# Kernel optimization log

Measured on AMD Instinct MI355X. Metric: run time of the kernel, lower is better.

Reference implementation:

```python
import jax, jax.numpy as jnp
import numpy as np

N = 50000          # nodes
E = 800000         # edges (avg degree 16)
INPUT_DIM = 1024
K = 10             # conv1d kernel
STRIDE = 8
COUT = (INPUT_DIM - K) // STRIDE + 1   # 127, matches floor formula
H = 256            # hidden_dim


def setup_inputs() -> dict:
    key = jax.random.key(0)
    ks = jax.random.split(key, 12)
    sc = lambda k, s: (jax.random.normal(k, s, jnp.float32) * 0.05)
    inp = {}
    inp["h"] = jax.random.normal(ks[0], (N, INPUT_DIM), jnp.float32)
    inp["src"] = jax.random.randint(ks[1], (E,), 0, N, dtype=jnp.int32)
    inp["dst"] = jax.random.randint(ks[2], (E,), 0, N, dtype=jnp.int32)
    # Conv1d(1,1,k=10,stride=8)
    inp["conv1d_w"] = sc(ks[3], (1, 1, K))
    inp["conv1d_b"] = jnp.zeros((1,), jnp.float32)
    # SAGEConv1: 127 -> 256 (mean aggregator: fc_self + fc_neigh)
    inp["w_self1"] = sc(ks[4], (COUT, H))
    inp["w_neigh1"] = sc(ks[5], (COUT, H))
    inp["b1"] = jnp.zeros((H,), jnp.float32)
    # SAGEConv2: 256 -> 128
    inp["w_self2"] = sc(ks[6], (H, H // 2))
    inp["w_neigh2"] = sc(ks[7], (H, H // 2))
    inp["b2"] = jnp.zeros((H // 2,), jnp.float32)
    # MLP head 128 -> 64 -> 32 -> 1
    inp["fc1_w"] = sc(ks[8], (H // 2, H // 4)); inp["fc1_b"] = jnp.zeros((H // 4,), jnp.float32)
    inp["fc2_w"] = sc(ks[9], (H // 4, H // 8)); inp["fc2_b"] = jnp.zeros((H // 8,), jnp.float32)
    inp["fc3_w"] = sc(ks[10], (H // 8, 1));    inp["fc3_b"] = jnp.zeros((1,), jnp.float32)
    return inp


def _sage_mean(x, src, dst, w_self, w_neigh, b):
    # mean over in-neighbors (src -> dst), zero for isolated nodes (DGL semantics)
    ones = jnp.ones((src.shape[0],), x.dtype)
    deg = jax.ops.segment_sum(ones, dst, num_segments=N)          # [N]
    agg = jax.ops.segment_sum(x[src], dst, num_segments=N)        # [N, F]
    agg = agg / jnp.maximum(deg, 1.0)[:, None]
    return x @ w_self + agg @ w_neigh + b


def reference(h, src, dst, conv1d_w, conv1d_b,
              w_self1, w_neigh1, b1, w_self2, w_neigh2, b2,
              fc1_w, fc1_b, fc2_w, fc2_b, fc3_w, fc3_b):
    # per-node 1D conv over feature axis: [N,1,1024] -> [N,1,127]
    x = jax.lax.conv_general_dilated(h[:, None, :], conv1d_w, (STRIDE,), 'VALID',
                                     dimension_numbers=('NCH', 'OIH', 'NCH'))
    x = jax.nn.relu(x[:, 0, :] + conv1d_b)                        # [N, 127]
    x = jax.nn.relu(_sage_mean(x, src, dst, w_self1, w_neigh1, b1))  # [N, 256]
    x = jax.nn.relu(_sage_mean(x, src, dst, w_self2, w_neigh2, b2))  # [N, 128]
    hg = jnp.mean(x, axis=0, keepdims=True)                       # AvgPooling -> [1, 128]
    y = jax.nn.relu(hg @ fc1_w + fc1_b)
    y = jax.nn.relu(y @ fc2_w + fc2_b)
    return y @ fc3_w + fc3_b                                      # [1, 1]
```

## Files before the change

kernel.cpp:

```cpp
#include <hip/hip_runtime.h>

#define N_NODES 50000
#define N_EDGES 800000
#define IN_DIM  1024
#define COUT    127
#define H1      256
#define H2      128
#define LDA     256
#define MBLK    391
#define NPART   4096
#define LDSS    72

typedef __bf16 bf16;
typedef __attribute__((ext_vector_type(8))) __bf16 bf16x8;
typedef __attribute__((ext_vector_type(4))) float floatx4;

__global__ void conv_kernel(const float* __restrict__ h, const float* __restrict__ w,
                            const float* __restrict__ b, bf16* __restrict__ xa) {
    int n = blockIdx.x;
    int t = threadIdx.x;
    const float* hr = h + (size_t)n * IN_DIM;
    float r = 0.f;
    if (t < COUT) {
        const float* p = hr + t * 8;
        float4 a = *(const float4*)p;
        float4 c = *(const float4*)(p + 4);
        float2 d = *(const float2*)(p + 8);
        float s = b[0];
        s += a.x * w[0] + a.y * w[1] + a.z * w[2] + a.w * w[3];
        s += c.x * w[4] + c.y * w[5] + c.z * w[6] + c.w * w[7];
        s += d.x * w[8] + d.y * w[9];
        r = fmaxf(s, 0.f);
    }
    xa[(size_t)n * LDA + t] = (bf16)r;
}

__global__ void deg_kernel(const int* __restrict__ dst, int* __restrict__ deg) {
    int e = blockIdx.x * blockDim.x + threadIdx.x;
    if (e < N_EDGES) atomicAdd(&deg[dst[e]], 1);
}

__global__ __launch_bounds__(1024) void scan_kernel(const int* __restrict__ deg,
                                                    int* __restrict__ rowptr,
                                                    int* __restrict__ cursor) {
    __shared__ int wsum[16];
    __shared__ int carry_s;
    int tid = threadIdx.x;
    int lane = tid & 63, wid = tid >> 6;
    if (tid == 0) carry_s = 0;
    __syncthreads();
    for (int base = 0; base < N_NODES; base += 1024) {
        int i = base + tid;
        int v = (i < N_NODES) ? deg[i] : 0;
        int s = v;
        #pragma unroll
        for (int off = 1; off < 64; off <<= 1) {
            int t = __shfl_up(s, off);
            if (lane >= off) s += t;
        }
        if (lane == 63) wsum[wid] = s;
        __syncthreads();
        if (tid < 16) {
            int ws = wsum[tid];
            #pragma unroll
            for (int off = 1; off < 16; off <<= 1) {
                int t = __shfl_up(ws, off);
                if (tid >= off) ws += t;
            }
            wsum[tid] = ws;
        }
        __syncthreads();
        int wpre = (wid == 0) ? 0 : wsum[wid - 1];
        int excl = carry_s + wpre + (s - v);
        if (i < N_NODES) { rowptr[i] = excl; cursor[i] = excl; }
        int tot = wsum[15];
        __syncthreads();
        if (tid == 0) carry_s += tot;
        __syncthreads();
    }
    if (tid == 0) rowptr[N_NODES] = carry_s;
}

__global__ void fill_kernel(const int* __restrict__ src, const int* __restrict__ dst,
                            int* __restrict__ cursor, int* __restrict__ esrc) {
    int e = blockIdx.x * blockDim.x + threadIdx.x;
    if (e < N_EDGES) {
        int d = dst[e];
        int pos = atomicAdd(&cursor[d], 1);
        esrc[pos] = src[e];
    }
}

__global__ void agg_kernel(bf16* __restrict__ xa, const int* __restrict__ rowptr,
                           const int* __restrict__ esrc) {
    int n = blockIdx.x;
    int f = threadIdx.x;
    int s0 = rowptr[n], s1 = rowptr[n + 1];
    float acc = 0.f;
    int e = s0;
    for (; e + 8 <= s1; e += 8) {
        int i0 = esrc[e],     i1 = esrc[e + 1], i2 = esrc[e + 2], i3 = esrc[e + 3];
        int i4 = esrc[e + 4], i5 = esrc[e + 5], i6 = esrc[e + 6], i7 = esrc[e + 7];
        float v0 = (float)xa[(size_t)i0 * LDA + f];
        float v1 = (float)xa[(size_t)i1 * LDA + f];
        float v2 = (float)xa[(size_t)i2 * LDA + f];
        float v3 = (float)xa[(size_t)i3 * LDA + f];
        float v4 = (float)xa[(size_t)i4 * LDA + f];
        float v5 = (float)xa[(size_t)i5 * LDA + f];
        float v6 = (float)xa[(size_t)i6 * LDA + f];
        float v7 = (float)xa[(size_t)i7 * LDA + f];
        acc += ((v0 + v1) + (v2 + v3)) + ((v4 + v5) + (v6 + v7));
    }
    for (; e < s1; ++e) acc += (float)xa[(size_t)esrc[e] * LDA + f];
    float dnm = (float)max(s1 - s0, 1);
    xa[(size_t)n * LDA + 128 + f] = (bf16)(acc / dnm);
}

__global__ void padw1_kernel(const float* __restrict__ ws, const float* __restrict__ wn,
                             bf16* __restrict__ wt) {
    int i = blockIdx.x * blockDim.x + threadIdx.x;
    int n = i >> 8, k = i & 255;
    float v = 0.f;
    if (k < COUT)                      v = ws[k * H1 + n];
    else if (k >= 128 && k < 128 + COUT) v = wn[(k - 128) * H1 + n];
    wt[i] = (bf16)v;
}

__global__ void padw2_kernel(const float* __restrict__ ws, const float* __restrict__ wn,
                             bf16* __restrict__ wt) {
    int i = blockIdx.x * blockDim.x + threadIdx.x;
    int n = i >> 8, k = i & 255;
    float v = (n < H2) ? ws[k * H2 + n] : wn[k * H2 + (n - H2)];
    wt[i] = (bf16)v;
}

template <bool RELU>
__global__ __launch_bounds__(256) void gemm_mfma(
        const bf16* __restrict__ X, const bf16* __restrict__ WT,
        const float* __restrict__ bias, bf16* __restrict__ out) {
    __shared__ bf16 As[128 * LDSS];
    __shared__ bf16 Bs[64 * LDSS];
    int tid  = threadIdx.x;
    int lane = tid & 63, w = tid >> 6;
    int quad = lane >> 4, l16 = lane & 15;
    int m0 = blockIdx.x * 128;
    int n0 = blockIdx.y * 64;
    floatx4 acc[2][4] = {};

    for (int k0 = 0; k0 < 256; k0 += 64) {
        uint4 av[4], bv[2];
        #pragma unroll
        for (int i = 0; i < 4; ++i) {
            int c = tid + 256 * i;
            int row = c >> 3, col = (c & 7) * 8;
            int gr = m0 + row;
            av[i] = (gr < N_NODES) ? *(const uint4*)(X + (size_t)gr * LDA + k0 + col)
                                   : make_uint4(0u, 0u, 0u, 0u);
        }
        #pragma unroll
        for (int i = 0; i < 2; ++i) {
            int c = tid + 256 * i;
            int row = c >> 3, col = (c & 7) * 8;
            bv[i] = *(const uint4*)(WT + (size_t)(n0 + row) * 256 + k0 + col);
        }
        __syncthreads();
        #pragma unroll
        for (int i = 0; i < 4; ++i) {
            int c = tid + 256 * i;
            int row = c >> 3, col = (c & 7) * 8;
            *(uint4*)&As[row * LDSS + col] = av[i];
        }
        #pragma unroll
        for (int i = 0; i < 2; ++i) {
            int c = tid + 256 * i;
            int row = c >> 3, col = (c & 7) * 8;
            *(uint4*)&Bs[row * LDSS + col] = bv[i];
        }
        __syncthreads();

        #pragma unroll
        for (int ks = 0; ks < 2; ++ks) {
            int kin = ks * 32 + quad * 8;
            bf16x8 a0 = *(const bf16x8*)&As[(w * 32 + l16) * LDSS + kin];
            bf16x8 a1 = *(const bf16x8*)&As[(w * 32 + 16 + l16) * LDSS + kin];
            bf16x8 b0 = *(const bf16x8*)&Bs[(l16) * LDSS + kin];
            bf16x8 b1 = *(const bf16x8*)&Bs[(16 + l16) * LDSS + kin];
            bf16x8 b2 = *(const bf16x8*)&Bs[(32 + l16) * LDSS + kin];
            bf16x8 b3 = *(const bf16x8*)&Bs[(48 + l16) * LDSS + kin];
            acc[0][0] = __builtin_amdgcn_mfma_f32_16x16x32_bf16(a0, b0, acc[0][0], 0, 0, 0);
            acc[0][1] = __builtin_amdgcn_mfma_f32_16x16x32_bf16(a0, b1, acc[0][1], 0, 0, 0);
            acc[0][2] = __builtin_amdgcn_mfma_f32_16x16x32_bf16(a0, b2, acc[0][2], 0, 0, 0);
            acc[0][3] = __builtin_amdgcn_mfma_f32_16x16x32_bf16(a0, b3, acc[0][3], 0, 0, 0);
            acc[1][0] = __builtin_amdgcn_mfma_f32_16x16x32_bf16(a1, b0, acc[1][0], 0, 0, 0);
            acc[1][1] = __builtin_amdgcn_mfma_f32_16x16x32_bf16(a1, b1, acc[1][1], 0, 0, 0);
            acc[1][2] = __builtin_amdgcn_mfma_f32_16x16x32_bf16(a1, b2, acc[1][2], 0, 0, 0);
            acc[1][3] = __builtin_amdgcn_mfma_f32_16x16x32_bf16(a1, b3, acc[1][3], 0, 0, 0);
        }
    }

    float bvv[4] = {};
    if constexpr (RELU) {
        #pragma unroll
        for (int nt = 0; nt < 4; ++nt) bvv[nt] = bias[n0 + nt * 16 + l16];
    }
    #pragma unroll
    for (int mt = 0; mt < 2; ++mt) {
        #pragma unroll
        for (int r = 0; r < 4; ++r) {
            int m = m0 + w * 32 + mt * 16 + quad * 4 + r;
            if (m < N_NODES) {
                #pragma unroll
                for (int nt = 0; nt < 4; ++nt) {
                    float v = acc[mt][nt][r];
                    if constexpr (RELU) v = fmaxf(v + bvv[nt], 0.f);
                    out[(size_t)m * LDA + n0 + nt * 16 + l16] = (bf16)v;
                }
            }
        }
    }
}

__global__ __launch_bounds__(128) void agg_epi_kernel(
        const bf16* __restrict__ P, const int* __restrict__ rowptr,
        const int* __restrict__ esrc, const float* __restrict__ b2,
        float* __restrict__ partial) {
    int f = threadIdx.x;
    float bf = b2[f];
    float csum = 0.f;
    for (int n = blockIdx.x; n < N_NODES; n += gridDim.x) {
        int s0 = rowptr[n], s1 = rowptr[n + 1];
        float acc = 0.f;
        int e = s0;
        for (; e + 8 <= s1; e += 8) {
            int i0 = esrc[e],     i1 = esrc[e + 1], i2 = esrc[e + 2], i3 = esrc[e + 3];
            int i4 = esrc[e + 4], i5 = esrc[e + 5], i6 = esrc[e + 6], i7 = esrc[e + 7];
            float v0 = (float)P[(size_t)i0 * LDA + H2 + f];
            float v1 = (float)P[(size_t)i1 * LDA + H2 + f];
            float v2 = (float)P[(size_t)i2 * LDA + H2 + f];
            float v3 = (float)P[(size_t)i3 * LDA + H2 + f];
            float v4 = (float)P[(size_t)i4 * LDA + H2 + f];
            float v5 = (float)P[(size_t)i5 * LDA + H2 + f];
            float v6 = (float)P[(size_t)i6 * LDA + H2 + f];
            float v7 = (float)P[(size_t)i7 * LDA + H2 + f];
            acc += ((v0 + v1) + (v2 + v3)) + ((v4 + v5) + (v6 + v7));
        }
        for (; e < s1; ++e) acc += (float)P[(size_t)esrc[e] * LDA + H2 + f];
        float dnm = (float)max(s1 - s0, 1);
        float y = (float)P[(size_t)n * LDA + f] + acc / dnm + bf;
        csum += fmaxf(y, 0.f);
    }
    partial[(size_t)blockIdx.x * 128 + f] = csum;
}

__global__ __launch_bounds__(256) void reduce_kernel(const float* __restrict__ partial,
                                                     float* __restrict__ hg) {
    int f = blockIdx.x, t = threadIdx.x;
    float s = 0.f;
    for (int i = t; i < NPART; i += 256) s += partial[(size_t)i * 128 + f];
    __shared__ float ls[4];
    #pragma unroll
    for (int off = 32; off >= 1; off >>= 1) s += __shfl_down(s, off);
    if ((t & 63) == 0) ls[t >> 6] = s;
    __syncthreads();
    if (t == 0) hg[f] = (ls[0] + ls[1]) + (ls[2] + ls[3]);
}

__global__ void mlp_kernel(const float* __restrict__ hg,
                           const float* __restrict__ f1w, const float* __restrict__ f1b,
                           const float* __restrict__ f2w, const float* __restrict__ f2b,
                           const float* __restrict__ f3w, const float* __restrict__ f3b,
                           float* __restrict__ out) {
    __shared__ float h0[128], y1[64], y2[32];
    int t = threadIdx.x;
    if (t < 128) h0[t] = hg[t] * (1.0f / N_NODES);
    __syncthreads();
    if (t < 64) {
        float s = f1b[t];
        for (int k = 0; k < 128; ++k) s += h0[k] * f1w[k * 64 + t];
        y1[t] = fmaxf(s, 0.f);
    }
    __syncthreads();
    if (t < 32) {
        float s = f2b[t];
        for (int k = 0; k < 64; ++k) s += y1[k] * f2w[k * 32 + t];
        y2[t] = fmaxf(s, 0.f);
    }
    __syncthreads();
    if (t == 0) {
        float s = f3b[0];
        for (int k = 0; k < 32; ++k) s += y2[k] * f3w[k];
        out[0] = s;
    }
}

extern "C" void kernel_launch(void* const* d_in, const int* in_sizes, int n_in,
                              void* d_out, int out_size, void* d_ws, size_t ws_size,
                              hipStream_t stream) {
    (void)in_sizes; (void)n_in; (void)out_size; (void)ws_size;
    const float* h        = (const float*)d_in[0];
    const int*   src      = (const int*)d_in[1];
    const int*   dst      = (const int*)d_in[2];
    const float* cw       = (const float*)d_in[3];
    const float* cb       = (const float*)d_in[4];
    const float* w_self1  = (const float*)d_in[5];
    const float* w_neigh1 = (const float*)d_in[6];
    const float* b1       = (const float*)d_in[7];
    const float* w_self2  = (const float*)d_in[8];
    const float* w_neigh2 = (const float*)d_in[9];
    const float* b2       = (const float*)d_in[10];
    const float* f1w      = (const float*)d_in[11];
    const float* f1b      = (const float*)d_in[12];
    const float* f2w      = (const float*)d_in[13];
    const float* f2b      = (const float*)d_in[14];
    const float* f3w      = (const float*)d_in[15];
    const float* f3b      = (const float*)d_in[16];
    float* out = (float*)d_out;

    char* ws = (char*)d_ws;
    bf16*  xa    = (bf16*) (ws + 0);
    bf16*  P     = (bf16*) (ws + 0);
    bf16*  x2    = (bf16*) (ws + 25624576);
    bf16*  wt1   = (bf16*) (ws + 51249152);
    bf16*  wt2   = (bf16*) (ws + 51380224);
    int*   deg   = (int*)  (ws + 51511296);
    int*   rowp  = (int*)  (ws + 51711488);
    int*   esrc  = (int*)  (ws + 51911936);
    float* part  = (float*)(ws + 55111936);
    float* hg    = (float*)(ws + 57209088);
    int*   cur   = deg;

    hipMemsetAsync(deg, 0, N_NODES * sizeof(int), stream);

    padw1_kernel<<<256, 256, 0, stream>>>(w_self1, w_neigh1, wt1);
    padw2_kernel<<<256, 256, 0, stream>>>(w_self2, w_neigh2, wt2);
    deg_kernel<<<(N_EDGES + 255) / 256, 256, 0, stream>>>(dst, deg);
    scan_kernel<<<1, 1024, 0, stream>>>(deg, rowp, cur);
    fill_kernel<<<(N_EDGES + 255) / 256, 256, 0, stream>>>(src, dst, cur, esrc);
    conv_kernel<<<N_NODES, 128, 0, stream>>>(h, cw, cb, xa);
    agg_kernel<<<N_NODES, 128, 0, stream>>>(xa, rowp, esrc);
    dim3 g(MBLK, 4);
    gemm_mfma<true><<<g, 256, 0, stream>>>(xa, wt1, b1, x2);
    gemm_mfma<false><<<g, 256, 0, stream>>>(x2, wt2, nullptr, P);
    agg_epi_kernel<<<NPART, 128, 0, stream>>>(P, rowp, esrc, b2, part);
    reduce_kernel<<<128, 256, 0, stream>>>(part, hg);
    mlp_kernel<<<1, 128, 0, stream>>>(hg, f1w, f1b, f2w, f2b, f3w, f3b, out);
}
```

Before: 599.9 us.

## Vectorize gathers to bf16x2 per lane, persist conv, fuse padw+memset, vectorize scan

Both neighbor-aggregation kernels now assign one wavefront per node, with each lane loading a packed pair of bf16 values and unpacking them with bit operations. This halves the gather instruction count, and readfirstlane keeps the row bounds scalar. The conv kernel becomes grid-stride with weights held in registers. The two weight-padding kernels and the degree memset are merged into one launch, and the scan processes 8 elements per thread using int4 loads and stores. The partial-sum buffer grows to 8192 rows, so the hg offset in the workspace moves.

Result: faster. 553.1 us (-7.8%).

```diff
diff --git a/kernel.cpp b/kernel.cpp
--- a/kernel.cpp
+++ b/kernel.cpp
@@ -8,31 +8,63 @@
 #define H2      128
 #define LDA     256
 #define MBLK    391
-#define NPART   4096
+#define EPB     2048
+#define NROWS   8192
 #define LDSS    72
 
 typedef __bf16 bf16;
 typedef __attribute__((ext_vector_type(8))) __bf16 bf16x8;
+typedef __attribute__((ext_vector_type(2))) __bf16 bf16x2;
 typedef __attribute__((ext_vector_type(4))) float floatx4;
 
-__global__ void conv_kernel(const float* __restrict__ h, const float* __restrict__ w,
-                            const float* __restrict__ b, bf16* __restrict__ xa) {
-    int n = blockIdx.x;
-    int t = threadIdx.x;
-    const float* hr = h + (size_t)n * IN_DIM;
-    float r = 0.f;
-    if (t < COUT) {
-        const float* p = hr + t * 8;
-        float4 a = *(const float4*)p;
-        float4 c = *(const float4*)(p + 4);
-        float2 d = *(const float2*)(p + 8);
-        float s = b[0];
-        s += a.x * w[0] + a.y * w[1] + a.z * w[2] + a.w * w[3];
-        s += c.x * w[4] + c.y * w[5] + c.z * w[6] + c.w * w[7];
-        s += d.x * w[8] + d.y * w[9];
-        r = fmaxf(s, 0.f);
-    }
-    xa[(size_t)n * LDA + t] = (bf16)r;
+__device__ __forceinline__ float blo(unsigned int u) { return __uint_as_float(u << 16); }
+__device__ __forceinline__ float bhi(unsigned int u) { return __uint_as_float(u & 0xffff0000u); }
+
+__global__ __launch_bounds__(256) void conv_kernel(const float* __restrict__ h,
+                                                   const float* __restrict__ w,
+                                                   const float* __restrict__ b,
+                                                   bf16* __restrict__ xa) {
+    int t    = threadIdx.x & 127;
+    int half = threadIdx.x >> 7;
+    float wv[10];
+    #pragma unroll
+    for (int j = 0; j < 10; ++j) wv[j] = w[j];
+    float bb = b[0];
+    for (int n = blockIdx.x * 2 + half; n < N_NODES; n += gridDim.x * 2) {
+        const float* hr = h + (size_t)n * IN_DIM;
+        float r = 0.f;
+        if (t < COUT) {
+            const float* p = hr + t * 8;
+            float4 a = *(const float4*)p;
+            float4 c = *(const float4*)(p + 4);
+            float2 d = *(const float2*)(p + 8);
+            float s = bb;
+            s += a.x * wv[0] + a.y * wv[1] + a.z * wv[2] + a.w * wv[3];
+            s += c.x * wv[4] + c.y * wv[5] + c.z * wv[6] + c.w * wv[7];
+            s += d.x * wv[8] + d.y * wv[9];
+            r = fmaxf(s, 0.f);
+        }
+        xa[(size_t)n * LDA + t] = (bf16)r;
+    }
+}
+
+__global__ void padw_kernel(const float* __restrict__ ws1, const float* __restrict__ wn1,
+                            const float* __restrict__ ws2, const float* __restrict__ wn2,
+                            bf16* __restrict__ wt1, bf16* __restrict__ wt2,
+                            int* __restrict__ deg) {
+    int i = blockIdx.x * blockDim.x + threadIdx.x;
+    int j = i & 65535;
+    int n = j >> 8, k = j & 255;
+    if (i < 65536) {
+        float v = 0.f;
+        if (k < COUT)                        v = ws1[k * H1 + n];
+        else if (k >= 128 && k < 128 + COUT) v = wn1[(k - 128) * H1 + n];
+        wt1[j] = (bf16)v;
+    } else {
+        float v = (n < H2) ? ws2[k * H2 + n] : wn2[k * H2 + (n - H2)];
+        wt2[j] = (bf16)v;
+    }
+    if (i < 50048) deg[i] = 0;
 }
 
 __global__ void deg_kernel(const int* __restrict__ dst, int* __restrict__ deg) {
@@ -49,10 +81,22 @@
     int lane = tid & 63, wid = tid >> 6;
     if (tid == 0) carry_s = 0;
     __syncthreads();
-    for (int base = 0; base < N_NODES; base += 1024) {
-        int i = base + tid;
-        int v = (i < N_NODES) ? deg[i] : 0;
-        int s = v;
+    for (int base = 0; base < N_NODES; base += 8192) {
+        int i0 = base + tid * 8;
+        int v[8];
+        if (i0 + 8 <= N_NODES) {
+            int4 a = *(const int4*)&deg[i0];
+            int4 c = *(const int4*)&deg[i0 + 4];
+            v[0] = a.x; v[1] = a.y; v[2] = a.z; v[3] = a.w;
+            v[4] = c.x; v[5] = c.y; v[6] = c.z; v[7] = c.w;
+        } else {
+            #pragma unroll
+            for (int j = 0; j < 8; ++j) v[j] = (i0 + j < N_NODES) ? deg[i0 + j] : 0;
+        }
+        int p[8]; int run = 0;
+        #pragma unroll
+        for (int j = 0; j < 8; ++j) { run += v[j]; p[j] = run; }
+        int s = run;
         #pragma unroll
         for (int off = 1; off < 64; off <<= 1) {
             int t = __shfl_up(s, off);
@@ -70,9 +114,20 @@
             wsum[tid] = ws;
         }
         __syncthreads();
-        int wpre = (wid == 0) ? 0 : wsum[wid - 1];
-        int excl = carry_s + wpre + (s - v);
-        if (i < N_NODES) { rowptr[i] = excl; cursor[i] = excl; }
+        int wpre  = (wid == 0) ? 0 : wsum[wid - 1];
+        int excl0 = carry_s + wpre + (s - run);
+        int o[8];
+        #pragma unroll
+        for (int j = 0; j < 8; ++j) o[j] = excl0 + p[j] - v[j];
+        if (i0 + 8 <= N_NODES) {
+            *(int4*)&rowptr[i0]     = make_int4(o[0], o[1], o[2], o[3]);
+            *(int4*)&rowptr[i0 + 4] = make_int4(o[4], o[5], o[6], o[7]);
+            *(int4*)&cursor[i0]     = make_int4(o[0], o[1], o[2], o[3]);
+            *(int4*)&cursor[i0 + 4] = make_int4(o[4], o[5], o[6], o[7]);
+        } else {
+            for (int j = 0; j < 8; ++j)
+                if (i0 + j < N_NODES) { rowptr[i0 + j] = o[j]; cursor[i0 + j] = o[j]; }
+        }
         int tot = wsum[15];
         __syncthreads();
         if (tid == 0) carry_s += tot;
@@ -91,47 +146,41 @@
     }
 }
 
-__global__ void agg_kernel(bf16* __restrict__ xa, const int* __restrict__ rowptr,
-                           const int* __restrict__ esrc) {
-    int n = blockIdx.x;
-    int f = threadIdx.x;
-    int s0 = rowptr[n], s1 = rowptr[n + 1];
-    float acc = 0.f;
+__global__ __launch_bounds__(256) void agg_kernel(bf16* __restrict__ xa,
+                                                  const int* __restrict__ rowptr,
+                                                  const int* __restrict__ esrc) {
+    int lane = threadIdx.x & 63;
+    int w    = threadIdx.x >> 6;
+    int n    = blockIdx.x * 4 + w;
+    int s0 = __builtin_amdgcn_readfirstlane(rowptr[n]);
+    int s1 = __builtin_amdgcn_readfirstlane(rowptr[n + 1]);
+    float ax = 0.f, ay = 0.f;
     int e = s0;
     for (; e + 8 <= s1; e += 8) {
         int i0 = esrc[e],     i1 = esrc[e + 1], i2 = esrc[e + 2], i3 = esrc[e + 3];
         int i4 = esrc[e + 4], i5 = esrc[e + 5], i6 = esrc[e + 6], i7 = esrc[e + 7];
-        float v0 = (float)xa[(size_t)i0 * LDA + f];
-        float v1 = (float)xa[(size_t)i1 * LDA + f];
-        float v2 = (float)xa[(size_t)i2 * LDA + f];
-        float v3 = (float)xa[(size_t)i3 * LDA + f];
-        float v4 = (float)xa[(size_t)i4 * LDA + f];
-        float v5 = (float)xa[(size_t)i5 * LDA + f];
-        float v6 = (float)xa[(size_t)i6 * LDA + f];
-        float v7 = (float)xa[(size_t)i7 * LDA + f];
-        acc += ((v0 + v1) + (v2 + v3)) + ((v4 + v5) + (v6 + v7));
-    }
-    for (; e < s1; ++e) acc += (float)xa[(size_t)esrc[e] * LDA + f];
+        unsigned u0 = ((const unsigned*)(xa + (size_t)i0 * LDA))[lane];
+        unsigned u1 = ((const unsigned*)(xa + (size_t)i1 * LDA))[lane];
+        unsigned u2 = ((const unsigned*)(xa + (size_t)i2 * LDA))[lane];
+        unsigned u3 = ((const unsigned*)(xa + (size_t)i3 * LDA))[lane];
+        unsigned u4 = ((const unsigned*)(xa + (size_t)i4 * LDA))[lane];
+        unsigned u5 = ((const unsigned*)(xa + (size_t)i5 * LDA))[lane];
+        unsigned u6 = ((const unsigned*)(xa + (size_t)i6 * LDA))[lane];
+        unsigned u7 = ((const unsigned*)(xa + (size_t)i7 * LDA))[lane];
+        ax += ((blo(u0) + blo(u1)) + (blo(u2) + blo(u3)))
+            + ((blo(u4) + blo(u5)) + (blo(u6) + blo(u7)));
+        ay += ((bhi(u0) + bhi(u1)) + (bhi(u2) + bhi(u3)))
+            + ((bhi(u4) + bhi(u5)) + (bhi(u6) + bhi(u7)));
+    }
+    for (; e < s1; ++e) {
+        unsigned u = ((const unsigned*)(xa + (size_t)esrc[e] * LDA))[lane];
+        ax += blo(u); ay += bhi(u);
+    }
     float dnm = (float)max(s1 - s0, 1);
-    xa[(size_t)n * LDA + 128 + f] = (bf16)(acc / dnm);
-}
-
-__global__ void padw1_kernel(const float* __restrict__ ws, const float* __restrict__ wn,
-                             bf16* __restrict__ wt) {
-    int i = blockIdx.x * blockDim.x + threadIdx.x;
-    int n = i >> 8, k = i & 255;
-    float v = 0.f;
-    if (k < COUT)                      v = ws[k * H1 + n];
-    else if (k >= 128 && k < 128 + COUT) v = wn[(k - 128) * H1 + n];
-    wt[i] = (bf16)v;
-}
-
-__global__ void padw2_kernel(const float* __restrict__ ws, const float* __restrict__ wn,
-                             bf16* __restrict__ wt) {
-    int i = blockIdx.x * blockDim.x + threadIdx.x;
-    int n = i >> 8, k = i & 255;
-    float v = (n < H2) ? ws[k * H2 + n] : wn[k * H2 + (n - H2)];
-    wt[i] = (bf16)v;
+    bf16x2 o;
+    o[0] = (bf16)(ax / dnm);
+    o[1] = (bf16)(ay / dnm);
+    *(bf16x2*)(xa + (size_t)n * LDA + 128 + 2 * lane) = o;
 }
 
 template <bool RELU>
@@ -220,43 +269,55 @@
     }
 }
 
-__global__ __launch_bounds__(128) void agg_epi_kernel(
+__global__ __launch_bounds__(256) void agg_epi_kernel(
         const bf16* __restrict__ P, const int* __restrict__ rowptr,
         const int* __restrict__ esrc, const float* __restrict__ b2,
         float* __restrict__ partial) {
-    int f = threadIdx.x;
-    float bf = b2[f];
-    float csum = 0.f;
-    for (int n = blockIdx.x; n < N_NODES; n += gridDim.x) {
-        int s0 = rowptr[n], s1 = rowptr[n + 1];
-        float acc = 0.f;
+    int lane = threadIdx.x & 63;
+    int w    = threadIdx.x >> 6;
+    int wid  = blockIdx.x * 4 + w;
+    float2 bfv = *(const float2*)(b2 + 2 * lane);
+    float csx = 0.f, csy = 0.f;
+    for (int n = wid; n < N_NODES; n += 4 * gridDim.x) {
+        int s0 = __builtin_amdgcn_readfirstlane(rowptr[n]);
+        int s1 = __builtin_amdgcn_readfirstlane(rowptr[n + 1]);
+        float ax = 0.f, ay = 0.f;
         int e = s0;
         for (; e + 8 <= s1; e += 8) {
             int i0 = esrc[e],     i1 = esrc[e + 1], i2 = esrc[e + 2], i3 = esrc[e + 3];
             int i4 = esrc[e + 4], i5 = esrc[e + 5], i6 = esrc[e + 6], i7 = esrc[e + 7];
-            float v0 = (float)P[(size_t)i0 * LDA + H2 + f];
-            float v1 = (float)P[(size_t)i1 * LDA + H2 + f];
-            float v2 = (float)P[(size_t)i2 * LDA + H2 + f];
-            float v3 = (float)P[(size_t)i3 * LDA + H2 + f];
-            float v4 = (float)P[(size_t)i4 * LDA + H2 + f];
-            float v5 = (float)P[(size_t)i5 * LDA + H2 + f];
-            float v6 = (float)P[(size_t)i6 * LDA + H2 + f];
-            float v7 = (float)P[(size_t)i7 * LDA + H2 + f];
-            acc += ((v0 + v1) + (v2 + v3)) + ((v4 + v5) + (v6 + v7));
-        }
-        for (; e < s1; ++e) acc += (float)P[(size_t)esrc[e] * LDA + H2 + f];
+            unsigned u0 = ((const unsigned*)(P + (size_t)i0 * LDA + H2))[lane];
+            unsigned u1 = ((const unsigned*)(P + (size_t)i1 * LDA + H2))[lane];
+            unsigned u2 = ((const unsigned*)(P + (size_t)i2 * LDA + H2))[lane];
+            unsigned u3 = ((const unsigned*)(P + (size_t)i3 * LDA + H2))[lane];
+            unsigned u4 = ((const unsigned*)(P + (size_t)i4 * LDA + H2))[lane];
+            unsigned u5 = ((const unsigned*)(P + (size_t)i5 * LDA + H2))[lane];
+            unsigned u6 = ((const unsigned*)(P + (size_t)i6 * LDA + H2))[lane];
+            unsigned u7 = ((const unsigned*)(P + (size_t)i7 * LDA + H2))[lane];
+            ax += ((blo(u0) + blo(u1)) + (blo(u2) + blo(u3)))
+                + ((blo(u4) + blo(u5)) + (blo(u6) + blo(u7)));
+            ay += ((bhi(u0) + bhi(u1)) + (bhi(u2) + bhi(u3)))
+                + ((bhi(u4) + bhi(u5)) + (bhi(u6) + bhi(u7)));
+        }
+        for (; e < s1; ++e) {
+            unsigned u = ((const unsigned*)(P + (size_t)esrc[e] * LDA + H2))[lane];
+            ax += blo(u); ay += bhi(u);
+        }
         float dnm = (float)max(s1 - s0, 1);
-        float y = (float)P[(size_t)n * LDA + f] + acc / dnm + bf;
-        csum += fmaxf(y, 0.f);
-    }
-    partial[(size_t)blockIdx.x * 128 + f] = csum;
+        unsigned us = ((const unsigned*)(P + (size_t)n * LDA))[lane];
+        float yx = blo(us) + ax / dnm + bfv.x;
+        float yy = bhi(us) + ay / dnm + bfv.y;
+        csx += fmaxf(yx, 0.f);
+        csy += fmaxf(yy, 0.f);
+    }
+    *(float2*)(partial + (size_t)wid * 128 + 2 * lane) = make_float2(csx, csy);
 }
 
 __global__ __launch_bounds__(256) void reduce_kernel(const float* __restrict__ partial,
                                                      float* __restrict__ hg) {
     int f = blockIdx.x, t = threadIdx.x;
     float s = 0.f;
-    for (int i = t; i < NPART; i += 256) s += partial[(size_t)i * 128 + f];
+    for (int i = t; i < NROWS; i += 256) s += partial[(size_t)i * 128 + f];
     __shared__ float ls[4];
     #pragma unroll
     for (int off = 32; off >= 1; off >>= 1) s += __shfl_down(s, off);
@@ -326,22 +387,19 @@
     int*   rowp  = (int*)  (ws + 51711488);
     int*   esrc  = (int*)  (ws + 51911936);
     float* part  = (float*)(ws + 55111936);
-    float* hg    = (float*)(ws + 57209088);
+    float* hg    = (float*)(ws + 59306240);
     int*   cur   = deg;
 
-    hipMemsetAsync(deg, 0, N_NODES * sizeof(int), stream);
-
-    padw1_kernel<<<256, 256, 0, stream>>>(w_self1, w_neigh1, wt1);
-    padw2_kernel<<<256, 256, 0, stream>>>(w_self2, w_neigh2, wt2);
+    padw_kernel<<<512, 256, 0, stream>>>(w_self1, w_neigh1, w_self2, w_neigh2, wt1, wt2, deg);
     deg_kernel<<<(N_EDGES + 255) / 256, 256, 0, stream>>>(dst, deg);
     scan_kernel<<<1, 1024, 0, stream>>>(deg, rowp, cur);
     fill_kernel<<<(N_EDGES + 255) / 256, 256, 0, stream>>>(src, dst, cur, esrc);
-    conv_kernel<<<N_NODES, 128, 0, stream>>>(h, cw, cb, xa);
-    agg_kernel<<<N_NODES, 128, 0, stream>>>(xa, rowp, esrc);
+    conv_kernel<<<2048, 256, 0, stream>>>(h, cw, cb, xa);
+    agg_kernel<<<12500, 256, 0, stream>>>(xa, rowp, esrc);
     dim3 g(MBLK, 4);
     gemm_mfma<true><<<g, 256, 0, stream>>>(xa, wt1, b1, x2);
     gemm_mfma<false><<<g, 256, 0, stream>>>(x2, wt2, nullptr, P);
-    agg_epi_kernel<<<NPART, 128, 0, stream>>>(P, rowp, esrc, b2, part);
+    agg_epi_kernel<<<EPB, 256, 0, stream>>>(P, rowp, esrc, b2, part);
     reduce_kernel<<<128, 256, 0, stream>>>(part, hg);
     mlp_kernel<<<1, 128, 0, stream>>>(hg, f1w, f1b, f2w, f2b, f3w, f3b, out);
 }
```
